# Kernel tuning notes

Measured on AMD Instinct MI355X. Metric: run time of the kernel, lower is better.

Reference implementation:

```python
import jax, jax.numpy as jnp
import numpy as np

B, N = 2, 4096
BN_EPS = 1e-5
INV_STD = np.float32(1.0 / np.sqrt(1.0 + BN_EPS))  # BN inference: running_mean=0, running_var=1


def pconv(x, w):
    # 1x1 Conv1d == per-point matmul: x [B,C,N], w [Cout,Cin] -> [B,Cout,N]
    return jnp.einsum('oc,bcn->bon', w, x)


def bn(x, g, b):
    # inference BatchNorm1d with mean=0, var=1
    return x * (INV_STD * g)[None, :, None] + b[None, :, None]


def sa_layer(x, qk_w, v_w, v_b, t_w, t_b, g, b):
    # PCT offset-attention. q_conv and k_conv share weights, so energy is a Gram matrix.
    xq = pconv(x, qk_w)                                   # [B, C//2, N]
    energy = jnp.einsum('bcn,bcm->bnm', xq, xq)           # [B, N, N]
    att = jax.nn.softmax(energy, axis=-1)
    att = att / (1e-9 + att.sum(axis=1, keepdims=True))   # extra L1 renorm over dim=1
    xv = pconv(x, v_w) + v_b[None, :, None]               # [B, C, N]
    x_r = jnp.einsum('bcn,bnm->bcm', xv, att)             # [B, C, N]
    # offset=True branch
    x_r = jax.nn.relu(bn(pconv(x - x_r, t_w) + t_b[None, :, None], g, b))
    return x + x_r


def _forward(x, conv1_w, bn1_g, bn1_b, conv2_w, bn2_g, bn2_b, conv3_w, bn3_g, bn3_b,
             pt1_w, pt1_g, pt1_b, pt2_w, pt2_g, pt2_b,
             sa1_qk, sa1_vw, sa1_vb, sa1_tw, sa1_tb, sa1_g, sa1_b,
             sa2_qk, sa2_vw, sa2_vb, sa2_tw, sa2_tb, sa2_g, sa2_b,
             cf_w, cf_g, cf_b, s1_w, s1_g, s1_b, s2_w, s2_g, s2_b, s3_w):
    h = jnp.transpose(x, (0, 2, 1))                       # [B, 3, N]
    h = jax.nn.relu(bn(pconv(h, conv1_w), bn1_g, bn1_b))  # [B, 64, N]
    h = jax.nn.relu(bn(pconv(h, conv2_w), bn2_g, bn2_b))  # [B, 128, N]
    h = jax.nn.relu(bn(pconv(h, conv3_w), bn3_g, bn3_b))  # [B, 256, N]
    # Point_Transformer_Last
    h = jax.nn.relu(bn(pconv(h, pt1_w), pt1_g, pt1_b))
    h = jax.nn.relu(bn(pconv(h, pt2_w), pt2_g, pt2_b))
    x1 = sa_layer(h, sa1_qk, sa1_vw, sa1_vb, sa1_tw, sa1_tb, sa1_g, sa1_b)
    x2 = sa_layer(x1, sa2_qk, sa2_vw, sa2_vb, sa2_tw, sa2_tb, sa2_g, sa2_b)
    # original forward reuses sa2's weights for layers 3 and 4
    x3 = sa_layer(x2, sa2_qk, sa2_vw, sa2_vb, sa2_tw, sa2_tb, sa2_g, sa2_b)
    x4 = sa_layer(x3, sa2_qk, sa2_vw, sa2_vb, sa2_tw, sa2_tb, sa2_g, sa2_b)
    h = jnp.concatenate([x1, x2, x3, x4], axis=1)         # [B, 1024, N]
    face = jax.nn.leaky_relu(bn(pconv(h, cf_w), cf_g, cf_b), 0.2)  # [B, 512, N]
    gmax = jnp.max(face, axis=2, keepdims=True)           # adaptive_max_pool1d(.,1)
    h = jnp.concatenate([face, jnp.broadcast_to(gmax, face.shape)], axis=1)  # [B, 1024, N]
    h = jax.nn.leaky_relu(bn(pconv(h, s1_w), s1_g, s1_b), 0.2)
    h = jax.nn.leaky_relu(bn(pconv(h, s2_w), s2_g, s2_b), 0.2)
    h = pconv(h, s3_w)                                    # [B, 50, N]
    return jnp.transpose(h, (0, 2, 1))                    # [B, N, 50]


def setup_inputs() -> dict:
    key = jax.random.key(0)
    kit = iter(jax.random.split(key, 80))
    def W(co, ci):
        return jax.random.normal(next(kit), (co, ci), dtype=jnp.float32) / np.float32(np.sqrt(ci))
    def G(c):
        return 1.0 + 0.1 * jax.random.normal(next(kit), (c,), dtype=jnp.float32)
    def Bv(c):
        return 0.1 * jax.random.normal(next(kit), (c,), dtype=jnp.float32)
    d = {}
    d['x'] = jax.random.normal(next(kit), (B, N, 3), dtype=jnp.float32)
    d['conv1_w'] = W(64, 3);   d['bn1_g'] = G(64);  d['bn1_b'] = Bv(64)
    d['conv2_w'] = W(128, 64); d['bn2_g'] = G(128); d['bn2_b'] = Bv(128)
    d['conv3_w'] = W(256, 128); d['bn3_g'] = G(256); d['bn3_b'] = Bv(256)
    d['pt1_w'] = W(256, 256); d['pt1_g'] = G(256); d['pt1_b'] = Bv(256)
    d['pt2_w'] = W(256, 256); d['pt2_g'] = G(256); d['pt2_b'] = Bv(256)
    for p in ('sa1', 'sa2'):
        d[p + '_qk'] = 0.1 * W(128, 256)  # small scale keeps softmax unsaturated
        d[p + '_vw'] = W(256, 256); d[p + '_vb'] = Bv(256)
        d[p + '_tw'] = W(256, 256); d[p + '_tb'] = Bv(256)
        d[p + '_g'] = G(256); d[p + '_b'] = Bv(256)
    d['cf_w'] = W(512, 1024); d['cf_g'] = G(512); d['cf_b'] = Bv(512)
    d['s1_w'] = W(512, 1024); d['s1_g'] = G(512); d['s1_b'] = Bv(512)
    d['s2_w'] = W(256, 512); d['s2_g'] = G(256); d['s2_b'] = Bv(256)
    d['s3_w'] = W(50, 256)
    return d


def reference(x, conv1_w, bn1_g, bn1_b, conv2_w, bn2_g, bn2_b, conv3_w, bn3_g, bn3_b,
              pt1_w, pt1_g, pt1_b, pt2_w, pt2_g, pt2_b,
              sa1_qk, sa1_vw, sa1_vb, sa1_tw, sa1_tb, sa1_g, sa1_b,
              sa2_qk, sa2_vw, sa2_vb, sa2_tw, sa2_tb, sa2_g, sa2_b,
              cf_w, cf_g, cf_b, s1_w, s1_g, s1_b, s2_w, s2_g, s2_b, s3_w):
    return _forward(x, conv1_w, bn1_g, bn1_b, conv2_w, bn2_g, bn2_b, conv3_w, bn3_g, bn3_b,
                    pt1_w, pt1_g, pt1_b, pt2_w, pt2_g, pt2_b,
                    sa1_qk, sa1_vw, sa1_vb, sa1_tw, sa1_tb, sa1_g, sa1_b,
                    sa2_qk, sa2_vw, sa2_vb, sa2_tw, sa2_tb, sa2_g, sa2_b,
                    cf_w, cf_g, cf_b, s1_w, s1_g, s1_b, s2_w, s2_g, s2_b, s3_w)
```

## Files before the change

### kernel.cpp

```cpp
#include <hip/hip_runtime.h>
#include <hip/hip_bf16.h>


#define NPTS 4096
#define BATCH 2
#define MSPLIT 4
#define RSSPLIT 8
static constexpr float INV_STD = 0.9999950000374997f;

__device__ __forceinline__ float bf2f(unsigned short u) {
    return __uint_as_float(((unsigned int)u) << 16);
}
__device__ __forceinline__ unsigned short f2bf(float f) {
    unsigned int x = __float_as_uint(f);
    unsigned int r = (x + 0x7FFFu + ((x >> 16) & 1u)) >> 16;
    return (unsigned short)r;
}

__device__ __forceinline__ void async16(const unsigned short* g, unsigned short* l)
{
    __builtin_amdgcn_global_load_lds(
        (const __attribute__((address_space(1))) unsigned int*)(const void*)g,
        (__attribute__((address_space(3))) unsigned int*)(void*)l,
        16, 0, 0);
}

typedef __attribute__((ext_vector_type(8))) short short8;
typedef __attribute__((ext_vector_type(4))) short s16x4;
typedef __attribute__((ext_vector_type(4))) float f32x4;

struct WSplit {
    const float* src[14];
    int n[14];
    long long off[14];
};

__global__ __launch_bounds__(256)
void presplit_k(WSplit d, unsigned short* __restrict__ wbuf)
{
    int wi = blockIdx.y;
    int i = blockIdx.x * 256 + threadIdx.x;
    int n = d.n[wi];
    if (i >= n) return;
    float v = d.src[wi][i];
    unsigned short h = f2bf(v);
    unsigned short* dst = wbuf + d.off[wi];
    dst[i] = h;
    dst[n + i] = f2bf(v - bf2f(h));
}

__device__ __forceinline__ void nt_epilogue(
    float y, int rg, int cg, int b, int Nb,
    const float* bias, int bias_mode,
    const float* bng, const float* bnb,
    const unsigned short* res, long long res_bs, int res_ld, long long res_po,
    int act, int out_mode,
    void* Cp, long long c_bs, int c_ld, long long c_po)
{
    if (bias) {
        if (bias_mode == 3)      y += bias[rg];
        else if (bias_mode == 2) y += bias[b * Nb + cg];
        else                     y += bias[cg];
    }
    if (bng) y = y * (INV_STD * bng[cg]) + bnb[cg];
    if (act == 1) y = fmaxf(y, 0.f);
    else if (act == 2) y = (y > 0.f) ? y : 0.2f * y;
    if (res) {
        long long ri_ = (long long)b * res_bs + (long long)rg * res_ld + cg;
        y += bf2f(res[ri_]) + bf2f(res[res_po + ri_]);
    }
    long long ci = (long long)b * c_bs + (long long)rg * c_ld + cg;
    if (out_mode == 0) {
        unsigned short* C = (unsigned short*)Cp;
        unsigned short h = f2bf(y);
        C[ci] = h;
        C[c_po + ci] = f2bf(y - bf2f(h));
    } else if (out_mode == 1) {
        ((unsigned short*)Cp)[ci] = f2bf(y);
    } else {
        if (cg < Nb) ((float*)Cp)[ci] = y;
    }
}

__global__ __launch_bounds__(256)
void gemm_nt_split(const unsigned short* __restrict__ A, long long a_bs, int a_lda, long long a_po,
                   const unsigned short* __restrict__ B, long long b_bs, int b_lda, long long b_po,
                   void* __restrict__ Cp, long long c_bs, int c_ld, long long c_po,
                   int Nb, int K,
                   const float* __restrict__ bias, int bias_mode,
                   const float* __restrict__ bng, const float* __restrict__ bnb,
                   const unsigned short* __restrict__ res, long long res_bs, int res_ld, long long res_po,
                   int act, int out_mode)
{
    __shared__ unsigned short As[2][64 * 64];
    __shared__ unsigned short Bs[2][64 * 64];
    const int gx = gridDim.x, gy = gridDim.y;
    const int nblk = gx * gy * (int)gridDim.z;
    int d_ = blockIdx.x + gx * (blockIdx.y + gy * blockIdx.z);
    int w_ = (nblk & 7) ? d_ : ((d_ & 7) * (nblk >> 3) + (d_ >> 3));
    const int b = w_ / (gx * gy);
    const int rem_ = w_ % (gx * gy);
    const int m0 = (rem_ / gx) * 64, n0 = (rem_ % gx) * 64;
    const int t = threadIdx.x;
    const int lane = t & 63, w = t >> 6;
    const int wr = (w >> 1) * 32, wc = (w & 1) * 32;
    const int ml = lane & 15, q = lane >> 4;

    f32x4 acc[2][2] = {};

    for (int k0 = 0; k0 < K; k0 += 64) {
        __syncthreads();
        #pragma unroll
        for (int e = 0; e < 2; e++) {
            int idx = t + e * 256;
            int row = idx >> 3, blk = idx & 7;
            int gblk = blk ^ (row & 7);
            int lofs = (e * 256 + (t & 192)) * 8;
            const unsigned short* sA = A + (long long)b * a_bs
                                     + (long long)(m0 + row) * a_lda + k0 + gblk * 8;
            const unsigned short* sB = B + (long long)b * b_bs
                                     + (long long)(n0 + row) * b_lda + k0 + gblk * 8;
            async16(sA,        &As[0][0] + lofs);
            async16(sA + a_po, &As[1][0] + lofs);
            async16(sB,        &Bs[0][0] + lofs);
            async16(sB + b_po, &Bs[1][0] + lofs);
        }
        __syncthreads();
        #pragma unroll
        for (int kk = 0; kk < 2; kk++) {
            short8 ah[2], al[2], bh[2], bl[2];
            #pragma unroll
            for (int it = 0; it < 2; it++) {
                int row = wr + it * 16 + ml;
                int slot = (kk * 4 + q) ^ (row & 7);
                ah[it] = *(const short8*)(&As[0][row * 64 + slot * 8]);
                al[it] = *(const short8*)(&As[1][row * 64 + slot * 8]);
            }
            #pragma unroll
            for (int jt = 0; jt < 2; jt++) {
                int row = wc + jt * 16 + ml;
                int slot = (kk * 4 + q) ^ (row & 7);
                bh[jt] = *(const short8*)(&Bs[0][row * 64 + slot * 8]);
                bl[jt] = *(const short8*)(&Bs[1][row * 64 + slot * 8]);
            }
            #pragma unroll
            for (int it = 0; it < 2; it++)
                #pragma unroll
                for (int jt = 0; jt < 2; jt++) {
                    acc[it][jt] = __builtin_amdgcn_mfma_f32_16x16x32_bf16(ah[it], bh[jt], acc[it][jt], 0, 0, 0);
                    acc[it][jt] = __builtin_amdgcn_mfma_f32_16x16x32_bf16(ah[it], bl[jt], acc[it][jt], 0, 0, 0);
                    acc[it][jt] = __builtin_amdgcn_mfma_f32_16x16x32_bf16(al[it], bh[jt], acc[it][jt], 0, 0, 0);
                }
        }
    }

    #pragma unroll
    for (int it = 0; it < 2; it++)
        #pragma unroll
        for (int jt = 0; jt < 2; jt++)
            #pragma unroll
            for (int r = 0; r < 4; r++)
                nt_epilogue(acc[it][jt][r], m0 + wr + it * 16 + q * 4 + r,
                            n0 + wc + jt * 16 + ml, b, Nb,
                            bias, bias_mode, bng, bnb, res, res_bs, res_ld, res_po,
                            act, out_mode, Cp, c_bs, c_ld, c_po);
}

__global__ __launch_bounds__(256)
void gemm_nt_splitB(const unsigned short* __restrict__ A, long long a_bs, int a_lda, long long a_po,
                    const unsigned short* __restrict__ B, long long b_bs, int b_lda, long long b_po,
                    void* __restrict__ Cp, long long c_bs, int c_ld, long long c_po,
                    int Nb, int K,
                    const float* __restrict__ bias, int bias_mode,
                    const float* __restrict__ bng, const float* __restrict__ bnb,
                    const unsigned short* __restrict__ res, long long res_bs, int res_ld, long long res_po,
                    int act, int out_mode)
{
    __shared__ unsigned short As[2][2][64 * 64];
    __shared__ unsigned short Bs[2][2][64 * 64];
    const int gx = gridDim.x, gy = gridDim.y;
    const int nblk = gx * gy * (int)gridDim.z;
    int d_ = blockIdx.x + gx * (blockIdx.y + gy * blockIdx.z);
    int w_ = (nblk & 7) ? d_ : ((d_ & 7) * (nblk >> 3) + (d_ >> 3));
    const int b = w_ / (gx * gy);
    const int rem_ = w_ % (gx * gy);
    const int m0 = (rem_ / gx) * 64, n0 = (rem_ % gx) * 64;
    const int t = threadIdx.x;
    const int lane = t & 63, w = t >> 6;
    const int wr = (w >> 1) * 32, wc = (w & 1) * 32;
    const int ml = lane & 15, q = lane >> 4;

    f32x4 acc[2][2] = {};

    for (int k0 = 0; k0 < K; k0 += 128) {
        __syncthreads();
        #pragma unroll
        for (int sub = 0; sub < 2; sub++) {
            int kb = k0 + sub * 64;
            #pragma unroll
            for (int e = 0; e < 2; e++) {
                int idx = t + e * 256;
                int row = idx >> 3, blk = idx & 7;
                int gblk = blk ^ (row & 7);
                int lofs = (e * 256 + (t & 192)) * 8;
                const unsigned short* sA = A + (long long)b * a_bs
                                         + (long long)(m0 + row) * a_lda + kb + gblk * 8;
                const unsigned short* sB = B + (long long)b * b_bs
                                         + (long long)(n0 + row) * b_lda + kb + gblk * 8;
                async16(sA,        &As[0][sub][0] + lofs);
                async16(sA + a_po, &As[1][sub][0] + lofs);
                async16(sB,        &Bs[0][sub][0] + lofs);
                async16(sB + b_po, &Bs[1][sub][0] + lofs);
            }
        }
        __syncthreads();
        #pragma unroll
        for (int sub = 0; sub < 2; sub++)
            #pragma unroll
            for (int kk = 0; kk < 2; kk++) {
                short8 ah[2], al[2], bh[2], bl[2];
                #pragma unroll
                for (int it = 0; it < 2; it++) {
                    int row = wr + it * 16 + ml;
                    int slot = (kk * 4 + q) ^ (row & 7);
                    ah[it] = *(const short8*)(&As[0][sub][row * 64 + slot * 8]);
                    al[it] = *(const short8*)(&As[1][sub][row * 64 + slot * 8]);
                }
                #pragma unroll
                for (int jt = 0; jt < 2; jt++) {
                    int row = wc + jt * 16 + ml;
                    int slot = (kk * 4 + q) ^ (row & 7);
                    bh[jt] = *(const short8*)(&Bs[0][sub][row * 64 + slot * 8]);
                    bl[jt] = *(const short8*)(&Bs[1][sub][row * 64 + slot * 8]);
                }
                #pragma unroll
                for (int it = 0; it < 2; it++)
                    #pragma unroll
                    for (int jt = 0; jt < 2; jt++) {
                        acc[it][jt] = __builtin_amdgcn_mfma_f32_16x16x32_bf16(ah[it], bh[jt], acc[it][jt], 0, 0, 0);
                        acc[it][jt] = __builtin_amdgcn_mfma_f32_16x16x32_bf16(ah[it], bl[jt], acc[it][jt], 0, 0, 0);
                        acc[it][jt] = __builtin_amdgcn_mfma_f32_16x16x32_bf16(al[it], bh[jt], acc[it][jt], 0, 0, 0);
                    }
            }
    }

    #pragma unroll
    for (int it = 0; it < 2; it++)
        #pragma unroll
        for (int jt = 0; jt < 2; jt++)
            #pragma unroll
            for (int r = 0; r < 4; r++)
                nt_epilogue(acc[it][jt][r], m0 + wr + it * 16 + q * 4 + r,
                            n0 + wc + jt * 16 + ml, b, Nb,
                            bias, bias_mode, bng, bnb, res, res_bs, res_ld, res_po,
                            act, out_mode, Cp, c_bs, c_ld, c_po);
}

__global__ __launch_bounds__(256)
void gemm_nt_split3(const unsigned short* __restrict__ A, long long a_bs, int a_lda, long long a_po,
                    const unsigned short* __restrict__ B, long long b_bs, int b_lda, long long b_po,
                    void* __restrict__ Cp, long long c_bs, int c_ld, long long c_po,
                    int Nb, int K,
                    const float* __restrict__ bias, int bias_mode,
                    const float* __restrict__ bng, const float* __restrict__ bnb,
                    const unsigned short* __restrict__ res, long long res_bs, int res_ld, long long res_po,
                    int act, int out_mode)
{
    __shared__ unsigned short As[2][128 * 64];
    __shared__ unsigned short Bs[2][64 * 64];
    const int gx = gridDim.x, gy = gridDim.y;
    const int nblk = gx * gy * (int)gridDim.z;
    int d_ = blockIdx.x + gx * (blockIdx.y + gy * blockIdx.z);
    int w_ = (nblk & 7) ? d_ : ((d_ & 7) * (nblk >> 3) + (d_ >> 3));
    const int b = w_ / (gx * gy);
    const int rem_ = w_ % (gx * gy);
    const int m0 = (rem_ / gx) * 128, n0 = (rem_ % gx) * 64;
    const int t = threadIdx.x;
    const int lane = t & 63, w = t >> 6;
    const int wr = (w >> 1) * 64, wc = (w & 1) * 32;
    const int ml = lane & 15, q = lane >> 4;

    f32x4 acc[4][2] = {};

    for (int k0 = 0; k0 < K; k0 += 64) {
        __syncthreads();
        #pragma unroll
        for (int e = 0; e < 4; e++) {
            int idx = t + e * 256;
            int row = idx >> 3, blk = idx & 7;
            int gblk = blk ^ (row & 7);
            int lofs = (e * 256 + (t & 192)) * 8;
            const unsigned short* sA = A + (long long)b * a_bs
                                     + (long long)(m0 + row) * a_lda + k0 + gblk * 8;
            async16(sA,        &As[0][0] + lofs);
            async16(sA + a_po, &As[1][0] + lofs);
        }
        #pragma unroll
        for (int e = 0; e < 2; e++) {
            int idx = t + e * 256;
            int row = idx >> 3, blk = idx & 7;
            int gblk = blk ^ (row & 7);
            int lofs = (e * 256 + (t & 192)) * 8;
            const unsigned short* sB = B + (long long)b * b_bs
                                     + (long long)(n0 + row) * b_lda + k0 + gblk * 8;
            async16(sB,        &Bs[0][0] + lofs);
            async16(sB + b_po, &Bs[1][0] + lofs);
        }
        __syncthreads();
        #pragma unroll
        for (int kk = 0; kk < 2; kk++) {
            short8 ah[4], al[4], bh[2], bl[2];
            #pragma unroll
            for (int it = 0; it < 4; it++) {
                int row = wr + it * 16 + ml;
                int slot = (kk * 4 + q) ^ (row & 7);
                ah[it] = *(const short8*)(&As[0][row * 64 + slot * 8]);
                al[it] = *(const short8*)(&As[1][row * 64 + slot * 8]);
            }
            #pragma unroll
            for (int jt = 0; jt < 2; jt++) {
                int row = wc + jt * 16 + ml;
                int slot = (kk * 4 + q) ^ (row & 7);
                bh[jt] = *(const short8*)(&Bs[0][row * 64 + slot * 8]);
                bl[jt] = *(const short8*)(&Bs[1][row * 64 + slot * 8]);
            }
            #pragma unroll
            for (int it = 0; it < 4; it++)
                #pragma unroll
                for (int jt = 0; jt < 2; jt++) {
                    acc[it][jt] = __builtin_amdgcn_mfma_f32_16x16x32_bf16(ah[it], bh[jt], acc[it][jt], 0, 0, 0);
                    acc[it][jt] = __builtin_amdgcn_mfma_f32_16x16x32_bf16(ah[it], bl[jt], acc[it][jt], 0, 0, 0);
                    acc[it][jt] = __builtin_amdgcn_mfma_f32_16x16x32_bf16(al[it], bh[jt], acc[it][jt], 0, 0, 0);
                }
        }
    }

    #pragma unroll
    for (int it = 0; it < 4; it++)
        #pragma unroll
        for (int jt = 0; jt < 2; jt++)
            #pragma unroll
            for (int r = 0; r < 4; r++)
                nt_epilogue(acc[it][jt][r], m0 + wr + it * 16 + q * 4 + r,
                            n0 + wc + jt * 16 + ml, b, Nb,
                            bias, bias_mode, bng, bnb, res, res_bs, res_ld, res_po,
                            act, out_mode, Cp, c_bs, c_ld, c_po);
}

__global__ __launch_bounds__(256)
void rs_k(const unsigned short* __restrict__ xq, float* __restrict__ rs)
{
    __shared__ unsigned short Kq[2][2][64 * 64];
    int d_ = blockIdx.x + 8 * (blockIdx.y + 64 * blockIdx.z);
    int w_ = (d_ & 7) * 128 + (d_ >> 3);
    const int p0 = (w_ % 64) * 64;
    const int xseg = (w_ / 64) % 8;
    const int b = w_ / 512;
    const int m_beg = xseg * (NPTS / RSSPLIT);
    const unsigned short* xqB = xq + (long long)b * NPTS * 128;
    const int t = threadIdx.x;
    const int lane = t & 63, w = t >> 6;
    const int pw = w * 16;
    const int ml = lane & 15, q = lane >> 4;

    short8 af[4];
    #pragma unroll
    for (int ks = 0; ks < 4; ks++)
        af[ks] = *(const short8*)(xqB + (long long)(p0 + pw + ml) * 128 + ks * 32 + q * 8);

    float rsum[4] = {0.f, 0.f, 0.f, 0.f};

    auto stageK = [&](int m0, int buf) {
        #pragma unroll
        for (int e = 0; e < 4; e++) {
            int idx = t + e * 256;
            int sub = idx >> 9, row = (idx >> 3) & 63, blk = idx & 7;
            int gblk = blk ^ (row & 7);
            int lofs = (e * 256 + (t & 192)) * 8;
            async16(xqB + (long long)(m0 + row) * 128 + sub * 64 + gblk * 8,
                    &Kq[buf][0][0] + lofs);
        }
    };

    constexpr int NIT = (NPTS / RSSPLIT) / 64;
    stageK(m_beg, 0);
    __syncthreads();

    for (int it = 0; it < NIT; ++it) {
        const int m0 = m_beg + it * 64;
        const int cur = it & 1;
        if (it + 1 < NIT) stageK(m0 + 64, cur ^ 1);
        f32x4 acc[4] = {};
        #pragma unroll
        for (int ks = 0; ks < 4; ks++) {
            int kh = ks >> 1, kk = ks & 1;
            #pragma unroll
            for (int jt = 0; jt < 4; jt++) {
                int row = jt * 16 + ml;
                int slot = (kk * 4 + q) ^ (row & 7);
                short8 bf = *(const short8*)(&Kq[cur][kh][row * 64 + slot * 8]);
                acc[jt] = __builtin_amdgcn_mfma_f32_16x16x32_bf16(af[ks], bf, acc[jt], 0, 0, 0);
            }
        }
        #pragma unroll
        for (int jt = 0; jt < 4; jt++)
            #pragma unroll
            for (int r = 0; r < 4; r++)
                rsum[r] += __expf(acc[jt][r]);
        __syncthreads();
    }
    #pragma unroll
    for (int r = 0; r < 4; r++) {
        float s = rsum[r];
        s += __shfl_xor(s, 1); s += __shfl_xor(s, 2);
        s += __shfl_xor(s, 4); s += __shfl_xor(s, 8);
        if (ml == 0) atomicAdd(&rs[b * NPTS + p0 + pw + q * 4 + r], s);
    }
}

__global__ __launch_bounds__(256)
void attn_pv(const unsigned short* __restrict__ xq,
             const unsigned short* __restrict__ xv,
             const float* __restrict__ rs,
             float* __restrict__ part,
             float* __restrict__ csp)
{
    __shared__ unsigned short Kq[2][2][64 * 64];
    __shared__ unsigned short Vv[256 * 64];
    __shared__ unsigned short Pl[64][64];
    int d_ = blockIdx.y + 64 * blockIdx.z;
    int w_ = (d_ & 7) * 64 + (d_ >> 3);
    const int p0 = (w_ % 64) * 64;
    const int z = w_ / 64;
    const int b = z / MSPLIT, ms = z % MSPLIT;
    const unsigned short* xqB = xq + (long long)b * NPTS * 128;
    const unsigned short* xvB = xv + (long long)b * 256 * NPTS;
    const float* rsB = rs + b * NPTS;
    const int t = threadIdx.x;
    const int lane = t & 63, w = t >> 6;
    const int pw = w * 16;
    const int cw = w * 64;
    const int ml = lane & 15, q = lane >> 4;

    short8 af[4];
    #pragma unroll
    for (int ks = 0; ks < 4; ks++)
        af[ks] = *(const short8*)(xqB + (long long)(p0 + pw + ml) * 128 + ks * 32 + q * 8);

    f32x4 pv[4][4] = {};
    float csr[4] = {0.f, 0.f, 0.f, 0.f};

    auto stageK = [&](int m0, int buf) {
        #pragma unroll
        for (int e = 0; e < 4; e++) {
            int idx = t + e * 256;
            int sub = idx >> 9, row = (idx >> 3) & 63, blk = idx & 7;
            int gblk = blk ^ (row & 7);
            int lofs = (e * 256 + (t & 192)) * 8;
            async16(xqB + (long long)(m0 + row) * 128 + sub * 64 + gblk * 8,
                    &Kq[buf][0][0] + lofs);
        }
    };
    auto stageV = [&](int m0) {
        #pragma unroll
        for (int e = 0; e < 8; e++) {
            int idx = t + e * 256;
            int row = idx >> 3, blk = idx & 7;
            int gblk = blk ^ (row & 7);
            int lofs = (e * 256 + (t & 192)) * 8;
            async16(xvB + (long long)row * NPTS + m0 + gblk * 8, Vv + lofs);
        }
    };

    const int m_beg = ms * (NPTS / MSPLIT);
    constexpr int NIT = (NPTS / MSPLIT) / 64;
    stageK(m_beg, 0);
    __syncthreads();

    for (int it = 0; it < NIT; ++it) {
        const int m0 = m_beg + it * 64;
        const int cur = it & 1;
        __syncthreads();
        stageV(m0);
        if (it + 1 < NIT) stageK(m0 + 64, cur ^ 1);
        f32x4 acc[4] = {};
        #pragma unroll
        for (int ks = 0; ks < 4; ks++) {
            int kh = ks >> 1, kk = ks & 1;
            #pragma unroll
            for (int jt = 0; jt < 4; jt++) {
                int row = jt * 16 + ml;
                int slot = (kk * 4 + q) ^ (row & 7);
                short8 bf = *(const short8*)(&Kq[cur][kh][row * 64 + slot * 8]);
                acc[jt] = __builtin_amdgcn_mfma_f32_16x16x32_bf16(af[ks], bf, acc[jt], 0, 0, 0);
            }
        }
        #pragma unroll
        for (int jt = 0; jt < 4; jt++) {
            float rvm = 1.f / rsB[m0 + jt * 16 + ml];
            #pragma unroll
            for (int r = 0; r < 4; r++) {
                float pvv = __expf(acc[jt][r]) * rvm;
                csr[r] += pvv;
                int cs_ = ((2 * jt + (ml >> 3)) ^ ((2 * q + (r >> 1)) & 7)) * 8 + (ml & 7);
                Pl[pw + q * 4 + r][cs_] = f2bf(pvv);
            }
        }
        __syncthreads();
        #pragma unroll
        for (int kk = 0; kk < 2; kk++) {
            short8 ap[4];
            #pragma unroll
            for (int pst = 0; pst < 4; pst++)
                ap[pst] = *(const short8*)(&Pl[pst * 16 + ml]
                           [((4 * kk + q) ^ ((ml >> 1) & 7)) * 8]);
            #pragma unroll
            for (int jt = 0; jt < 4; jt++) {
                int row = cw + jt * 16 + ml;
                int slot = (kk * 4 + q) ^ (row & 7);
                short8 bv = *(const short8*)(&Vv[row * 64 + slot * 8]);
                #pragma unroll
                for (int pst = 0; pst < 4; pst++)
                    pv[pst][jt] = __builtin_amdgcn_mfma_f32_16x16x32_bf16(
                        ap[pst], bv, pv[pst][jt], 0, 0, 0);
            }
        }
    }
    #pragma unroll
    for (int r = 0; r < 4; r++) {
        float s = csr[r];
        s += __shfl_xor(s, 1); s += __shfl_xor(s, 2);
        s += __shfl_xor(s, 4); s += __shfl_xor(s, 8);
        if (ml == 0) csp[(long long)z * NPTS + p0 + pw + q * 4 + r] = s;
    }
    float* C = part + (long long)z * ((long long)NPTS * 256);
    #pragma unroll
    for (int pst = 0; pst < 4; pst++)
        #pragma unroll
        for (int jt = 0; jt < 4; jt++)
            #pragma unroll
            for (int r = 0; r < 4; r++) {
                int rg = p0 + pst * 16 + q * 4 + r;
                int cg = cw + jt * 16 + ml;
                C[(long long)rg * 256 + cg] = pv[pst][jt][r];
            }
}

__global__ __launch_bounds__(256)
void conv1_k(const float* __restrict__ x, const float* __restrict__ w,
             const float* __restrict__ g, const float* __restrict__ bb,
             unsigned short* __restrict__ h, long long h_po)
{
    int b = blockIdx.y;
    int p = blockIdx.x * 4 + (threadIdx.x >> 6);
    int c = threadIdx.x & 63;
    const float* xp = x + ((long long)b * NPTS + p) * 3;
    float y = xp[0] * w[c * 3] + xp[1] * w[c * 3 + 1] + xp[2] * w[c * 3 + 2];
    y = y * (INV_STD * g[c]) + bb[c];
    y = fmaxf(y, 0.f);
    long long i = ((long long)b * NPTS + p) * 64 + c;
    unsigned short hi = f2bf(y);
    h[i] = hi;
    h[h_po + i] = f2bf(y - bf2f(hi));
}

__global__ __launch_bounds__(256)
void zero_k(float* __restrict__ p, int n)
{
    int i = blockIdx.x * 256 + threadIdx.x;
    if (i < n) p[i] = 0.f;
}

__global__ __launch_bounds__(256)
void diff_k(const unsigned short* __restrict__ xin, long long x_bs, int x_ld, long long x_po,
            const float* __restrict__ part, const float* __restrict__ csp,
            unsigned short* __restrict__ d, long long d_po)
{
    long long i4 = ((long long)blockIdx.x * 256 + threadIdx.x) * 4;
    int b = blockIdx.y;
    int p = (int)(i4 >> 8), c = (int)(i4 & 255);
    long long xi = (long long)b * x_bs + (long long)p * x_ld + c;
    s16x4 xh = *(const s16x4*)(xin + xi);
    s16x4 xl = *(const s16x4*)(xin + x_po + xi);
    float xr0 = 0.f, xr1 = 0.f, xr2 = 0.f, xr3 = 0.f, den = 1e-9f;
    #pragma unroll
    for (int ks = 0; ks < MSPLIT; ks++) {
        int z = b * MSPLIT + ks;
        f32x4 pv = *(const f32x4*)(part + (long long)z * ((long long)NPTS * 256) + i4);
        xr0 += pv[0]; xr1 += pv[1]; xr2 += pv[2]; xr3 += pv[3];
        den += csp[(long long)z * NPTS + p];
    }
    float v0 = bf2f((unsigned short)xh[0]) + bf2f((unsigned short)xl[0]) - xr0 / den;
    float v1 = bf2f((unsigned short)xh[1]) + bf2f((unsigned short)xl[1]) - xr1 / den;
    float v2 = bf2f((unsigned short)xh[2]) + bf2f((unsigned short)xl[2]) - xr2 / den;
    float v3 = bf2f((unsigned short)xh[3]) + bf2f((unsigned short)xl[3]) - xr3 / den;
    long long di = (long long)b * NPTS * 256 + i4;
    s16x4 hh, ll;
    hh[0] = (short)f2bf(v0); ll[0] = (short)f2bf(v0 - bf2f((unsigned short)hh[0]));
    hh[1] = (short)f2bf(v1); ll[1] = (short)f2bf(v1 - bf2f((unsigned short)hh[1]));
    hh[2] = (short)f2bf(v2); ll[2] = (short)f2bf(v2 - bf2f((unsigned short)hh[2]));
    hh[3] = (short)f2bf(v3); ll[3] = (short)f2bf(v3 - bf2f((unsigned short)hh[3]));
    *(s16x4*)(d + di) = hh;
    *(s16x4*)(d + d_po + di) = ll;
}

__global__ __launch_bounds__(256)
void gmaxp_k(const unsigned short* __restrict__ face, long long f_po, float* __restrict__ pm)
{
    __shared__ float red[4][512];
    int b = blockIdx.z;
    int seg = blockIdx.y * 4 + blockIdx.x;
    int w = threadIdx.x >> 6, l = threadIdx.x & 63;
    float m8[8];
    #pragma unroll
    for (int k = 0; k < 8; k++) m8[k] = -3.4e38f;
    for (int jj = 0; jj < 16; jj++) {
        int i = seg * 64 + jj * 4 + w;
        long long off = ((long long)b * NPTS + i) * 512 + l * 8;
        short8 h = *(const short8*)(face + off);
        short8 lo = *(const short8*)(face + f_po + off);
        #pragma unroll
        for (int k = 0; k < 8; k++)
            m8[k] = fmaxf(m8[k], bf2f((unsigned short)h[k]) + bf2f((unsigned short)lo[k]));
    }
    #pragma unroll
    for (int k = 0; k < 8; k++) red[w][l * 8 + k] = m8[k];
    __syncthreads();
    for (int c = threadIdx.x; c < 512; c += 256) {
        float m = fmaxf(fmaxf(red[0][c], red[1][c]), fmaxf(red[2][c], red[3][c]));
        pm[((long long)b * 64 + seg) * 512 + c] = m;
    }
}

__global__ __launch_bounds__(256)
void bias2_k(const float* __restrict__ w, const float* __restrict__ pm, float* __restrict__ b2)
{
    __shared__ float gml[512];
    int b = blockIdx.y;
    for (int c = threadIdx.x; c < 512; c += 256) {
        float m = -3.4e38f;
        for (int ch = 0; ch < 64; ch++)
            m = fmaxf(m, pm[((long long)b * 64 + ch) * 512 + c]);
        gml[c] = m;
    }
    __syncthreads();
    int o = blockIdx.x * 256 + threadIdx.x;
    float s = 0.f;
    for (int c = 0; c < 512; c++) s += w[(long long)o * 1024 + 512 + c] * gml[c];
    b2[b * 512 + o] = s;
}

extern "C" void kernel_launch(void* const* d_in, const int* in_sizes, int n_in,
                              void* d_out, int out_size, void* d_ws, size_t ws_size,
                              hipStream_t stream)
{
    const float* x       = (const float*)d_in[0];
    const float* conv1_w = (const float*)d_in[1];
    const float* bn1_g   = (const float*)d_in[2];
    const float* bn1_b   = (const float*)d_in[3];
    const float* conv2_w = (const float*)d_in[4];
    const float* bn2_g   = (const float*)d_in[5];
    const float* bn2_b   = (const float*)d_in[6];
    const float* conv3_w = (const float*)d_in[7];
    const float* bn3_g   = (const float*)d_in[8];
    const float* bn3_b   = (const float*)d_in[9];
    const float* pt1_w   = (const float*)d_in[10];
    const float* pt1_g   = (const float*)d_in[11];
    const float* pt1_b   = (const float*)d_in[12];
    const float* pt2_w   = (const float*)d_in[13];
    const float* pt2_g   = (const float*)d_in[14];
    const float* pt2_b   = (const float*)d_in[15];
    const float* sa_qk[2] = {(const float*)d_in[16], (const float*)d_in[23]};
    const float* sa_vw[2] = {(const float*)d_in[17], (const float*)d_in[24]};
    const float* sa_vb[2] = {(const float*)d_in[18], (const float*)d_in[25]};
    const float* sa_tw[2] = {(const float*)d_in[19], (const float*)d_in[26]};
    const float* sa_tb[2] = {(const float*)d_in[20], (const float*)d_in[27]};
    const float* sa_g[2]  = {(const float*)d_in[21], (const float*)d_in[28]};
    const float* sa_b[2]  = {(const float*)d_in[22], (const float*)d_in[29]};
    const float* cf_w = (const float*)d_in[30];
    const float* cf_g = (const float*)d_in[31];
    const float* cf_b = (const float*)d_in[32];
    const float* s1_w = (const float*)d_in[33];
    const float* s1_g = (const float*)d_in[34];
    const float* s1_b = (const float*)d_in[35];
    const float* s2_w = (const float*)d_in[36];
    const float* s2_g = (const float*)d_in[37];
    const float* s2_b = (const float*)d_in[38];
    const float* s3_w = (const float*)d_in[39];

    char* base = (char*)d_ws;
    size_t off = 0;
    auto alloc = [&](size_t bytes) -> void* {
        void* p = base + off;
        off = (off + bytes + 255) & ~(size_t)255;
        return p;
    };
    const long long N = NPTS;
    const long long PO64   = (long long)BATCH * N * 64;
    const long long PO128  = (long long)BATCH * N * 128;
    const long long PO256  = (long long)BATCH * N * 256;
    const long long PO512  = (long long)BATCH * N * 512;
    const long long PO1024 = (long long)BATCH * N * 1024;

    unsigned short* S1  = (unsigned short*)alloc(2 * PO256 * 2);
    unsigned short* S2  = (unsigned short*)alloc(2 * PO256 * 2);
    unsigned short* Dv  = (unsigned short*)alloc(2 * PO256 * 2);
    unsigned short* cat = (unsigned short*)alloc(2 * PO1024 * 2);
    unsigned short* face = (unsigned short*)alloc(2 * PO512 * 2);
    unsigned short* xq  = (unsigned short*)alloc((size_t)BATCH * N * 128 * 2);
    unsigned short* xv  = (unsigned short*)alloc((size_t)BATCH * 256 * N * 2);
    unsigned short* s1b = (unsigned short*)alloc(2 * PO512 * 2);
    unsigned short* s2b = (unsigned short*)alloc(2 * PO256 * 2);
    float* part = (float*)alloc((size_t)BATCH * MSPLIT * N * 256 * 4);
    float* csp  = (float*)alloc((size_t)BATCH * MSPLIT * N * 4);
    float* rs = (float*)alloc((size_t)4 * BATCH * N * 4);
    float* pm = (float*)alloc((size_t)BATCH * 64 * 512 * 4);
    float* b2 = (float*)alloc((size_t)BATCH * 512 * 4);
    unsigned short* wb = (unsigned short*)alloc((size_t)3400000 * 2);

    WSplit wd;
    const float* wsrc[14] = {conv2_w, conv3_w, pt1_w, pt2_w, sa_qk[0], sa_qk[1],
                             sa_vw[0], sa_vw[1], sa_tw[0], sa_tw[1], cf_w, s1_w, s2_w, s3_w};
    int wn[14] = {128*64, 256*128, 256*256, 256*256, 128*256, 128*256,
                  256*256, 256*256, 256*256, 256*256, 512*1024, 512*1024, 256*512, 50*256};
    long long wo[14]; long long acc_ = 0;
    for (int i = 0; i < 14; i++) { wd.src[i] = wsrc[i]; wd.n[i] = wn[i]; wd.off[i] = acc_; wo[i] = acc_; acc_ += 2LL * wn[i]; }
    presplit_k<<<dim3((512*1024 + 255) / 256, 14), 256, 0, stream>>>(wd, wb);
    auto W = [&](int i) { return wb + wo[i]; };

    auto nt = [&](const unsigned short* A, long long a_bs, int a_lda, long long a_po,
                  const unsigned short* B, long long b_bs, int b_lda, long long b_po,
                  void* C, long long c_bs, int c_ld, long long c_po,
                  int Mrows, int Nb, int K,
                  const float* bias, int bias_mode,
                  const float* bng, const float* bnb,
                  const unsigned short* res, long long res_bs, int res_ld, long long res_po,
                  int act, int out_mode) {
        dim3 g((Nb + 63) / 64, Mrows / 64, BATCH);
        gemm_nt_split<<<g, 256, 0, stream>>>(A, a_bs, a_lda, a_po, B, b_bs, b_lda, b_po,
                                             C, c_bs, c_ld, c_po, Nb, K,
                                             bias, bias_mode, bng, bnb,
                                             res, res_bs, res_ld, res_po, act, out_mode);
    };
    auto ntB = [&](const unsigned short* A, long long a_bs, int a_lda, long long a_po,
                   const unsigned short* B, long long b_bs, int b_lda, long long b_po,
                   void* C, long long c_bs, int c_ld, long long c_po,
                   int Mrows, int Nb, int K,
                   const float* bias, int bias_mode,
                   const float* bng, const float* bnb,
                   const unsigned short* res, long long res_bs, int res_ld, long long res_po,
                   int act, int out_mode) {
        dim3 g((Nb + 63) / 64, Mrows / 64, BATCH);
        gemm_nt_splitB<<<g, 256, 0, stream>>>(A, a_bs, a_lda, a_po, B, b_bs, b_lda, b_po,
                                              C, c_bs, c_ld, c_po, Nb, K,
                                              bias, bias_mode, bng, bnb,
                                              res, res_bs, res_ld, res_po, act, out_mode);
    };
    auto nt3 = [&](const unsigned short* A, long long a_bs, int a_lda, long long a_po,
                   const unsigned short* B, long long b_bs, int b_lda, long long b_po,
                   void* C, long long c_bs, int c_ld, long long c_po,
                   int Mrows, int Nb, int K,
                   const float* bias, int bias_mode,
                   const float* bng, const float* bnb,
                   const unsigned short* res, long long res_bs, int res_ld, long long res_po,
                   int act, int out_mode) {
        dim3 g((Nb + 63) / 64, Mrows / 128, BATCH);
        gemm_nt_split3<<<g, 256, 0, stream>>>(A, a_bs, a_lda, a_po, B, b_bs, b_lda, b_po,
                                              C, c_bs, c_ld, c_po, Nb, K,
                                              bias, bias_mode, bng, bnb,
                                              res, res_bs, res_ld, res_po, act, out_mode);
    };

    conv1_k<<<dim3(NPTS / 4, BATCH), 256, 0, stream>>>(x, conv1_w, bn1_g, bn1_b, S1, PO64);
    zero_k<<<(4 * BATCH * NPTS + 255) / 256, 256, 0, stream>>>(rs, 4 * BATCH * NPTS);
    nt(S1, N * 64, 64, PO64,    W(0), 0, 64, wn[0],  S2, N * 128, 128, PO128,
       NPTS, 128, 64,  nullptr, 0, bn2_g, bn2_b, nullptr, 0, 0, 0, 1, 0);
    ntB(S2, N * 128, 128, PO128, W(1), 0, 128, wn[1], S1, N * 256, 256, PO256,
        NPTS, 256, 128, nullptr, 0, bn3_g, bn3_b, nullptr, 0, 0, 0, 1, 0);
    ntB(S1, N * 256, 256, PO256, W(2), 0, 256, wn[2], S2, N * 256, 256, PO256,
        NPTS, 256, 256, nullptr, 0, pt1_g, pt1_b, nullptr, 0, 0, 0, 1, 0);
    ntB(S2, N * 256, 256, PO256, W(3), 0, 256, wn[3], S1, N * 256, 256, PO256,
        NPTS, 256, 256, nullptr, 0, pt2_g, pt2_b, nullptr, 0, 0, 0, 1, 0);

    for (int i = 0; i < 4; i++) {
        int p = (i == 0) ? 0 : 1;
        const unsigned short* xin = (i == 0) ? S1 : cat + (size_t)(i - 1) * 256;
        long long xin_bs = (i == 0) ? N * 256 : N * 1024;
        int xin_ld = (i == 0) ? 256 : 1024;
        long long xin_po = (i == 0) ? PO256 : PO1024;
        float* rsL = rs + (size_t)i * BATCH * NPTS;

        ntB(xin, xin_bs, xin_ld, xin_po, W(4 + p), 0, 256, wn[4 + p],
            xq, N * 128, 128, 0, NPTS, 128, 256,
            nullptr, 0, nullptr, nullptr, nullptr, 0, 0, 0, 0, 1);
        ntB(W(6 + p), 0, 256, wn[6 + p], xin, xin_bs, xin_ld, xin_po,
            xv, 256 * N, NPTS, 0, 256, NPTS, 256,
            sa_vb[p], 3, nullptr, nullptr, nullptr, 0, 0, 0, 0, 1);
        rs_k<<<dim3(RSSPLIT, NPTS / 64, BATCH), 256, 0, stream>>>(xq, rsL);
        attn_pv<<<dim3(1, NPTS / 64, BATCH * MSPLIT), 256, 0, stream>>>(
            xq, xv, rsL, part, csp);
        diff_k<<<dim3(NPTS * 256 / 1024, BATCH), 256, 0, stream>>>(
            xin, xin_bs, xin_ld, xin_po, part, csp, Dv, PO256);
        ntB(Dv, N * 256, 256, PO256, W(8 + p), 0, 256, wn[8 + p],
            cat + (size_t)i * 256, N * 1024, 1024, PO1024,
            NPTS, 256, 256, sa_tb[p], 1, sa_g[p], sa_b[p],
            xin, xin_bs, xin_ld, xin_po, 1, 0);
    }

    nt3(cat, N * 1024, 1024, PO1024, W(10), 0, 1024, wn[10],
        face, N * 512, 512, PO512, NPTS, 512, 1024,
        nullptr, 0, cf_g, cf_b, nullptr, 0, 0, 0, 2, 0);
    gmaxp_k<<<dim3(4, 16, BATCH), 256, 0, stream>>>(face, PO512, pm);
    bias2_k<<<dim3(2, BATCH), 256, 0, stream>>>(s1_w, pm, b2);
    nt3(face, N * 512, 512, PO512, W(11), 0, 1024, wn[11],
        s1b, N * 512, 512, PO512, NPTS, 512, 512,
        b2, 2, s1_g, s1_b, nullptr, 0, 0, 0, 2, 0);
    ntB(s1b, N * 512, 512, PO512, W(12), 0, 512, wn[12],
        s2b, N * 256, 256, PO256, NPTS, 256, 512,
        nullptr, 0, s2_g, s2_b, nullptr, 0, 0, 0, 2, 0);
    ntB(s2b, N * 256, 256, PO256, W(13), 0, 256, wn[13],
        d_out, N * 50, 50, 0, NPTS, 50, 256,
        nullptr, 0, nullptr, nullptr, nullptr, 0, 0, 0, 0, 2);
}
```

Baseline: 725.5 us.

## Double-buffer LDS tiles in the split-bf16 NT GEMM and unify its two variants

Replaces the two split-bf16 GEMM kernels (single-stage K=64 and two-substage K=128) with one kernel that keeps two LDS buffers. It issues the async global-to-LDS loads for the next 64-wide K tile before running the MFMAs on the current tile, with one barrier per iteration. The goal is to hide global load latency behind MFMA work in all the pointwise-conv GEMMs, including conv2, which previously used the non-overlapped kernel. In exchange, every launch now uses the larger 64 KB LDS footprint, which can lower occupancy, notably for the small-K conv2 layer.

```diff
diff --git a/kernel.cpp b/kernel.cpp
--- a/kernel.cpp
+++ b/kernel.cpp
@@ -91,90 +91,6 @@
                    const float* __restrict__ bng, const float* __restrict__ bnb,
                    const unsigned short* __restrict__ res, long long res_bs, int res_ld, long long res_po,
                    int act, int out_mode)
-{
-    __shared__ unsigned short As[2][64 * 64];
-    __shared__ unsigned short Bs[2][64 * 64];
-    const int gx = gridDim.x, gy = gridDim.y;
-    const int nblk = gx * gy * (int)gridDim.z;
-    int d_ = blockIdx.x + gx * (blockIdx.y + gy * blockIdx.z);
-    int w_ = (nblk & 7) ? d_ : ((d_ & 7) * (nblk >> 3) + (d_ >> 3));
-    const int b = w_ / (gx * gy);
-    const int rem_ = w_ % (gx * gy);
-    const int m0 = (rem_ / gx) * 64, n0 = (rem_ % gx) * 64;
-    const int t = threadIdx.x;
-    const int lane = t & 63, w = t >> 6;
-    const int wr = (w >> 1) * 32, wc = (w & 1) * 32;
-    const int ml = lane & 15, q = lane >> 4;
-
-    f32x4 acc[2][2] = {};
-
-    for (int k0 = 0; k0 < K; k0 += 64) {
-        __syncthreads();
-        #pragma unroll
-        for (int e = 0; e < 2; e++) {
-            int idx = t + e * 256;
-            int row = idx >> 3, blk = idx & 7;
-            int gblk = blk ^ (row & 7);
-            int lofs = (e * 256 + (t & 192)) * 8;
-            const unsigned short* sA = A + (long long)b * a_bs
-                                     + (long long)(m0 + row) * a_lda + k0 + gblk * 8;
-            const unsigned short* sB = B + (long long)b * b_bs
-                                     + (long long)(n0 + row) * b_lda + k0 + gblk * 8;
-            async16(sA,        &As[0][0] + lofs);
-            async16(sA + a_po, &As[1][0] + lofs);
-            async16(sB,        &Bs[0][0] + lofs);
-            async16(sB + b_po, &Bs[1][0] + lofs);
-        }
-        __syncthreads();
-        #pragma unroll
-        for (int kk = 0; kk < 2; kk++) {
-            short8 ah[2], al[2], bh[2], bl[2];
-            #pragma unroll
-            for (int it = 0; it < 2; it++) {
-                int row = wr + it * 16 + ml;
-                int slot = (kk * 4 + q) ^ (row & 7);
-                ah[it] = *(const short8*)(&As[0][row * 64 + slot * 8]);
-                al[it] = *(const short8*)(&As[1][row * 64 + slot * 8]);
-            }
-            #pragma unroll
-            for (int jt = 0; jt < 2; jt++) {
-                int row = wc + jt * 16 + ml;
-                int slot = (kk * 4 + q) ^ (row & 7);
-                bh[jt] = *(const short8*)(&Bs[0][row * 64 + slot * 8]);
-                bl[jt] = *(const short8*)(&Bs[1][row * 64 + slot * 8]);
-            }
-            #pragma unroll
-            for (int it = 0; it < 2; it++)
-                #pragma unroll
-                for (int jt = 0; jt < 2; jt++) {
-                    acc[it][jt] = __builtin_amdgcn_mfma_f32_16x16x32_bf16(ah[it], bh[jt], acc[it][jt], 0, 0, 0);
-                    acc[it][jt] = __builtin_amdgcn_mfma_f32_16x16x32_bf16(ah[it], bl[jt], acc[it][jt], 0, 0, 0);
-                    acc[it][jt] = __builtin_amdgcn_mfma_f32_16x16x32_bf16(al[it], bh[jt], acc[it][jt], 0, 0, 0);
-                }
-        }
-    }
-
-    #pragma unroll
-    for (int it = 0; it < 2; it++)
-        #pragma unroll
-        for (int jt = 0; jt < 2; jt++)
-            #pragma unroll
-            for (int r = 0; r < 4; r++)
-                nt_epilogue(acc[it][jt][r], m0 + wr + it * 16 + q * 4 + r,
-                            n0 + wc + jt * 16 + ml, b, Nb,
-                            bias, bias_mode, bng, bnb, res, res_bs, res_ld, res_po,
-                            act, out_mode, Cp, c_bs, c_ld, c_po);
-}
-
-__global__ __launch_bounds__(256)
-void gemm_nt_splitB(const unsigned short* __restrict__ A, long long a_bs, int a_lda, long long a_po,
-                    const unsigned short* __restrict__ B, long long b_bs, int b_lda, long long b_po,
-                    void* __restrict__ Cp, long long c_bs, int c_ld, long long c_po,
-                    int Nb, int K,
-                    const float* __restrict__ bias, int bias_mode,
-                    const float* __restrict__ bng, const float* __restrict__ bnb,
-                    const unsigned short* __restrict__ res, long long res_bs, int res_ld, long long res_po,
-                    int act, int out_mode)
 {
     __shared__ unsigned short As[2][2][64 * 64];
     __shared__ unsigned short Bs[2][2][64 * 64];
@@ -190,58 +106,58 @@
     const int wr = (w >> 1) * 32, wc = (w & 1) * 32;
     const int ml = lane & 15, q = lane >> 4;
 
+    auto stage = [&](int k0, int buf) {
+        #pragma unroll
+        for (int e = 0; e < 2; e++) {
+            int idx = t + e * 256;
+            int row = idx >> 3, blk = idx & 7;
+            int gblk = blk ^ (row & 7);
+            int lofs = (e * 256 + (t & 192)) * 8;
+            const unsigned short* sA = A + (long long)b * a_bs
+                                     + (long long)(m0 + row) * a_lda + k0 + gblk * 8;
+            const unsigned short* sB = B + (long long)b * b_bs
+                                     + (long long)(n0 + row) * b_lda + k0 + gblk * 8;
+            async16(sA,        &As[buf][0][0] + lofs);
+            async16(sA + a_po, &As[buf][1][0] + lofs);
+            async16(sB,        &Bs[buf][0][0] + lofs);
+            async16(sB + b_po, &Bs[buf][1][0] + lofs);
+        }
+    };
+
     f32x4 acc[2][2] = {};
-
-    for (int k0 = 0; k0 < K; k0 += 128) {
+    const int NK = K >> 6;
+    stage(0, 0);
+
+    for (int ks = 0; ks < NK; ++ks) {
         __syncthreads();
-        #pragma unroll
-        for (int sub = 0; sub < 2; sub++) {
-            int kb = k0 + sub * 64;
-            #pragma unroll
-            for (int e = 0; e < 2; e++) {
-                int idx = t + e * 256;
-                int row = idx >> 3, blk = idx & 7;
-                int gblk = blk ^ (row & 7);
-                int lofs = (e * 256 + (t & 192)) * 8;
-                const unsigned short* sA = A + (long long)b * a_bs
-                                         + (long long)(m0 + row) * a_lda + kb + gblk * 8;
-                const unsigned short* sB = B + (long long)b * b_bs
-                                         + (long long)(n0 + row) * b_lda + kb + gblk * 8;
-                async16(sA,        &As[0][sub][0] + lofs);
-                async16(sA + a_po, &As[1][sub][0] + lofs);
-                async16(sB,        &Bs[0][sub][0] + lofs);
-                async16(sB + b_po, &Bs[1][sub][0] + lofs);
-            }
-        }
-        __syncthreads();
-        #pragma unroll
-        for (int sub = 0; sub < 2; sub++)
-            #pragma unroll
-            for (int kk = 0; kk < 2; kk++) {
-                short8 ah[2], al[2], bh[2], bl[2];
-                #pragma unroll
-                for (int it = 0; it < 2; it++) {
-                    int row = wr + it * 16 + ml;
-                    int slot = (kk * 4 + q) ^ (row & 7);
-                    ah[it] = *(const short8*)(&As[0][sub][row * 64 + slot * 8]);
-                    al[it] = *(const short8*)(&As[1][sub][row * 64 + slot * 8]);
-                }
+        if (ks + 1 < NK) stage((ks + 1) << 6, (ks + 1) & 1);
+        const int buf = ks & 1;
+        #pragma unroll
+        for (int kk = 0; kk < 2; kk++) {
+            short8 ah[2], al[2], bh[2], bl[2];
+            #pragma unroll
+            for (int it = 0; it < 2; it++) {
+                int row = wr + it * 16 + ml;
+                int slot = (kk * 4 + q) ^ (row & 7);
+                ah[it] = *(const short8*)(&As[buf][0][row * 64 + slot * 8]);
+                al[it] = *(const short8*)(&As[buf][1][row * 64 + slot * 8]);
+            }
+            #pragma unroll
+            for (int jt = 0; jt < 2; jt++) {
+                int row = wc + jt * 16 + ml;
+                int slot = (kk * 4 + q) ^ (row & 7);
+                bh[jt] = *(const short8*)(&Bs[buf][0][row * 64 + slot * 8]);
+                bl[jt] = *(const short8*)(&Bs[buf][1][row * 64 + slot * 8]);
+            }
+            #pragma unroll
+            for (int it = 0; it < 2; it++)
                 #pragma unroll
                 for (int jt = 0; jt < 2; jt++) {
-                    int row = wc + jt * 16 + ml;
-                    int slot = (kk * 4 + q) ^ (row & 7);
-                    bh[jt] = *(const short8*)(&Bs[0][sub][row * 64 + slot * 8]);
-                    bl[jt] = *(const short8*)(&Bs[1][sub][row * 64 + slot * 8]);
+                    acc[it][jt] = __builtin_amdgcn_mfma_f32_16x16x32_bf16(ah[it], bh[jt], acc[it][jt], 0, 0, 0);
+                    acc[it][jt] = __builtin_amdgcn_mfma_f32_16x16x32_bf16(ah[it], bl[jt], acc[it][jt], 0, 0, 0);
+                    acc[it][jt] = __builtin_amdgcn_mfma_f32_16x16x32_bf16(al[it], bh[jt], acc[it][jt], 0, 0, 0);
                 }
-                #pragma unroll
-                for (int it = 0; it < 2; it++)
-                    #pragma unroll
-                    for (int jt = 0; jt < 2; jt++) {
-                        acc[it][jt] = __builtin_amdgcn_mfma_f32_16x16x32_bf16(ah[it], bh[jt], acc[it][jt], 0, 0, 0);
-                        acc[it][jt] = __builtin_amdgcn_mfma_f32_16x16x32_bf16(ah[it], bl[jt], acc[it][jt], 0, 0, 0);
-                        acc[it][jt] = __builtin_amdgcn_mfma_f32_16x16x32_bf16(al[it], bh[jt], acc[it][jt], 0, 0, 0);
-                    }
-            }
+        }
     }
 
     #pragma unroll
@@ -728,21 +644,7 @@
     presplit_k<<<dim3((512*1024 + 255) / 256, 14), 256, 0, stream>>>(wd, wb);
     auto W = [&](int i) { return wb + wo[i]; };
 
-    auto nt = [&](const unsigned short* A, long long a_bs, int a_lda, long long a_po,
-                  const unsigned short* B, long long b_bs, int b_lda, long long b_po,
-                  void* C, long long c_bs, int c_ld, long long c_po,
-                  int Mrows, int Nb, int K,
-                  const float* bias, int bias_mode,
-                  const float* bng, const float* bnb,
-                  const unsigned short* res, long long res_bs, int res_ld, long long res_po,
-                  int act, int out_mode) {
-        dim3 g((Nb + 63) / 64, Mrows / 64, BATCH);
-        gemm_nt_split<<<g, 256, 0, stream>>>(A, a_bs, a_lda, a_po, B, b_bs, b_lda, b_po,
-                                             C, c_bs, c_ld, c_po, Nb, K,
-                                             bias, bias_mode, bng, bnb,
-                                             res, res_bs, res_ld, res_po, act, out_mode);
-    };
-    auto ntB = [&](const unsigned short* A, long long a_bs, int a_lda, long long a_po,
+    auto ntU = [&](const unsigned short* A, long long a_bs, int a_lda, long long a_po,
                    const unsigned short* B, long long b_bs, int b_lda, long long b_po,
                    void* C, long long c_bs, int c_ld, long long c_po,
                    int Mrows, int Nb, int K,
@@ -751,10 +653,10 @@
                    const unsigned short* res, long long res_bs, int res_ld, long long res_po,
                    int act, int out_mode) {
         dim3 g((Nb + 63) / 64, Mrows / 64, BATCH);
-        gemm_nt_splitB<<<g, 256, 0, stream>>>(A, a_bs, a_lda, a_po, B, b_bs, b_lda, b_po,
-                                              C, c_bs, c_ld, c_po, Nb, K,
-                                              bias, bias_mode, bng, bnb,
-                                              res, res_bs, res_ld, res_po, act, out_mode);
+        gemm_nt_split<<<g, 256, 0, stream>>>(A, a_bs, a_lda, a_po, B, b_bs, b_lda, b_po,
+                                             C, c_bs, c_ld, c_po, Nb, K,
+                                             bias, bias_mode, bng, bnb,
+                                             res, res_bs, res_ld, res_po, act, out_mode);
     };
     auto nt3 = [&](const unsigned short* A, long long a_bs, int a_lda, long long a_po,
                    const unsigned short* B, long long b_bs, int b_lda, long long b_po,
@@ -773,13 +675,13 @@
 
     conv1_k<<<dim3(NPTS / 4, BATCH), 256, 0, stream>>>(x, conv1_w, bn1_g, bn1_b, S1, PO64);
     zero_k<<<(4 * BATCH * NPTS + 255) / 256, 256, 0, stream>>>(rs, 4 * BATCH * NPTS);
-    nt(S1, N * 64, 64, PO64,    W(0), 0, 64, wn[0],  S2, N * 128, 128, PO128,
-       NPTS, 128, 64,  nullptr, 0, bn2_g, bn2_b, nullptr, 0, 0, 0, 1, 0);
-    ntB(S2, N * 128, 128, PO128, W(1), 0, 128, wn[1], S1, N * 256, 256, PO256,
+    ntU(S1, N * 64, 64, PO64,    W(0), 0, 64, wn[0],  S2, N * 128, 128, PO128,
+        NPTS, 128, 64,  nullptr, 0, bn2_g, bn2_b, nullptr, 0, 0, 0, 1, 0);
+    ntU(S2, N * 128, 128, PO128, W(1), 0, 128, wn[1], S1, N * 256, 256, PO256,
         NPTS, 256, 128, nullptr, 0, bn3_g, bn3_b, nullptr, 0, 0, 0, 1, 0);
-    ntB(S1, N * 256, 256, PO256, W(2), 0, 256, wn[2], S2, N * 256, 256, PO256,
+    ntU(S1, N * 256, 256, PO256, W(2), 0, 256, wn[2], S2, N * 256, 256, PO256,
         NPTS, 256, 256, nullptr, 0, pt1_g, pt1_b, nullptr, 0, 0, 0, 1, 0);
-    ntB(S2, N * 256, 256, PO256, W(3), 0, 256, wn[3], S1, N * 256, 256, PO256,
+    ntU(S2, N * 256, 256, PO256, W(3), 0, 256, wn[3], S1, N * 256, 256, PO256,
         NPTS, 256, 256, nullptr, 0, pt2_g, pt2_b, nullptr, 0, 0, 0, 1, 0);
 
     for (int i = 0; i < 4; i++) {
@@ -790,10 +692,10 @@
         long long xin_po = (i == 0) ? PO256 : PO1024;
         float* rsL = rs + (size_t)i * BATCH * NPTS;
 
-        ntB(xin, xin_bs, xin_ld, xin_po, W(4 + p), 0, 256, wn[4 + p],
+        ntU(xin, xin_bs, xin_ld, xin_po, W(4 + p), 0, 256, wn[4 + p],
             xq, N * 128, 128, 0, NPTS, 128, 256,
             nullptr, 0, nullptr, nullptr, nullptr, 0, 0, 0, 0, 1);
-        ntB(W(6 + p), 0, 256, wn[6 + p], xin, xin_bs, xin_ld, xin_po,
+        ntU(W(6 + p), 0, 256, wn[6 + p], xin, xin_bs, xin_ld, xin_po,
             xv, 256 * N, NPTS, 0, 256, NPTS, 256,
             sa_vb[p], 3, nullptr, nullptr, nullptr, 0, 0, 0, 0, 1);
         rs_k<<<dim3(RSSPLIT, NPTS / 64, BATCH), 256, 0, stream>>>(xq, rsL);
@@ -801,7 +703,7 @@
             xq, xv, rsL, part, csp);
         diff_k<<<dim3(NPTS * 256 / 1024, BATCH), 256, 0, stream>>>(
             xin, xin_bs, xin_ld, xin_po, part, csp, Dv, PO256);
-        ntB(Dv, N * 256, 256, PO256, W(8 + p), 0, 256, wn[8 + p],
+        ntU(Dv, N * 256, 256, PO256, W(8 + p), 0, 256, wn[8 + p],
             cat + (size_t)i * 256, N * 1024, 1024, PO1024,
             NPTS, 256, 256, sa_tb[p], 1, sa_g[p], sa_b[p],
             xin, xin_bs, xin_ld, xin_po, 1, 0);
@@ -815,10 +717,10 @@
     nt3(face, N * 512, 512, PO512, W(11), 0, 1024, wn[11],
         s1b, N * 512, 512, PO512, NPTS, 512, 512,
         b2, 2, s1_g, s1_b, nullptr, 0, 0, 0, 2, 0);
-    ntB(s1b, N * 512, 512, PO512, W(12), 0, 512, wn[12],
+    ntU(s1b, N * 512, 512, PO512, W(12), 0, 512, wn[12],
         s2b, N * 256, 256, PO256, NPTS, 256, 512,
         nullptr, 0, s2_g, s2_b, nullptr, 0, 0, 0, 2, 0);
-    ntB(s2b, N * 256, 256, PO256, W(13), 0, 256, wn[13],
+    ntU(s2b, N * 256, 256, PO256, W(13), 0, 256, wn[13],
         d_out, N * 50, 50, 0, NPTS, 50, 256,
         nullptr, 0, nullptr, nullptr, nullptr, 0, 0, 0, 0, 2);
 }
```

Result: no change. 727.9 us (+0.3%).
